# Kernel tuning notes

Hardware: AMD Instinct MI355X
Metric: run time of the kernel (lower is better)

Reference implementation:

```python
import jax, jax.numpy as jnp
import numpy as np

B, T, C = 4, 2048, 1024
H = 16
D = C // H  # head_dim = 64

def setup_inputs() -> dict:
    key = jax.random.key(0)
    ks = jax.random.split(key, 5)
    scale = 0.02
    x = jax.random.normal(ks[0], (B, T, C), dtype=jnp.float32)
    # weights stored [in, out] (transpose of torch Linear layout; same math)
    Wqkv = jax.random.normal(ks[1], (C, 3 * C), dtype=jnp.float32) * scale
    bqkv = jnp.zeros((3 * C,), dtype=jnp.float32)
    Wproj = jax.random.normal(ks[2], (C, C), dtype=jnp.float32) * scale
    bproj = jnp.zeros((C,), dtype=jnp.float32)
    return {"x": x, "Wqkv": Wqkv, "bqkv": bqkv, "Wproj": Wproj, "bproj": bproj}

def reference(x, Wqkv, bqkv, Wproj, bproj):
    Bx, Tx, Cx = x.shape
    qkv = x @ Wqkv + bqkv                      # [B,T,3C]
    q, k, v = jnp.split(qkv, 3, axis=2)
    # [B,T,C] -> [B,H,T,D]
    q = q.reshape(Bx, Tx, H, D).transpose(0, 2, 1, 3)
    k = k.reshape(Bx, Tx, H, D).transpose(0, 2, 1, 3)
    v = v.reshape(Bx, Tx, H, D).transpose(0, 2, 1, 3)
    att = jnp.einsum('bhqd,bhkd->bhqk', q, k) / jnp.sqrt(jnp.float32(D))
    causal = jnp.tril(jnp.ones((Tx, Tx), dtype=bool))
    att = jnp.where(causal, att, jnp.float32(-jnp.inf))
    att = jax.nn.softmax(att, axis=-1)
    y = jnp.einsum('bhqk,bhkd->bhqd', att, v)  # [B,H,T,D]
    y = y.transpose(0, 2, 1, 3).reshape(Bx, Tx, Cx)
    return y @ Wproj + bproj
```

## Files before the change

### kernel.cpp

```cpp
#include <hip/hip_runtime.h>
#include <math.h>

#define Bb 4
#define Tt 2048
#define Cc 1024
#define Hh 16
#define Dd 64
#define QSC 0.18033688011112042f

typedef unsigned short ushort_t;
typedef __attribute__((ext_vector_type(8))) short short8;
typedef __attribute__((ext_vector_type(4))) float floatx4;

typedef unsigned int __attribute__((address_space(1))) u32_as1;
typedef unsigned int __attribute__((address_space(3))) u32_as3;

__device__ __forceinline__ void gld_lds16(const void* g, const void* lds_uniform) {
    __builtin_amdgcn_global_load_lds(
        (const u32_as1*)(unsigned long long)g,
        (u32_as3*)(unsigned int)(unsigned long long)lds_uniform,
        16, 0, 0);
}

__device__ inline ushort_t f2bf(float x) {
    unsigned int u = __float_as_uint(x);
    return (ushort_t)((u + 0x7FFFu + ((u >> 16) & 1u)) >> 16);
}

__device__ __forceinline__ void bar() {
    asm volatile("" ::: "memory");
    __builtin_amdgcn_s_barrier();
    asm volatile("" ::: "memory");
}

__global__ __launch_bounds__(256) void convert_kernel(
    const float* __restrict__ in, ushort_t* __restrict__ out, int n4)
{
    int i = blockIdx.x * 256 + threadIdx.x;
    if (i < n4) {
        float4 v = *(const float4*)&in[i * 4];
        ushort_t o[4] = {f2bf(v.x), f2bf(v.y), f2bf(v.z), f2bf(v.w)};
        *(uint2*)&out[i * 4] = *(uint2*)o;
    }
}

__global__ __launch_bounds__(256) void transpose_kernel(
    const float* __restrict__ W, ushort_t* __restrict__ Wt, int K, int N)
{
    __shared__ ushort_t Ts[16][72];
    const int n0 = blockIdx.x * 64;
    const int k0 = blockIdx.y * 16;
    const int t = threadIdx.x;
#pragma unroll
    for (int i = 0; i < 4; i++) {
        int e = t + i * 256;
        int kl = e >> 6, nl = e & 63;
        Ts[kl][nl] = f2bf(W[(size_t)(k0 + kl) * N + n0 + nl]);
    }
    __syncthreads();
    {
        int nl = t >> 2, kl4 = (t & 3) * 4;
        ushort_t o[4] = {Ts[kl4][nl], Ts[kl4 + 1][nl], Ts[kl4 + 2][nl], Ts[kl4 + 3][nl]};
        *(uint2*)&Wt[(size_t)(n0 + nl) * K + k0 + kl4] = *(uint2*)o;
    }
}

template <bool OUT_BF16, bool SCALE_Q>
__global__ __launch_bounds__(512) void gemm256_kernel(
    const ushort_t* __restrict__ A, const ushort_t* __restrict__ Bt,
    const float* __restrict__ bias, void* __restrict__ Co,
    int M, int N, int K)
{
    __shared__ __align__(16) ushort_t Ls[65536];

    const int tid = threadIdx.x;
    const int lane = tid & 63;
    const int w = tid >> 6;
    const int wm = w >> 2, wn = w & 3;
    const int l = lane & 15, q = lane >> 4;
    const int NT = K >> 6;

    const int n0 = blockIdx.x * 256;
    const int m0 = blockIdx.y * 256;

    const int ln = lane ^ (((lane >> 5) & 1) << 1);
    const ushort_t* Ag = A  + (size_t)(m0 + w * 16 + (ln >> 2)) * K + (ln & 3) * 8;
    const ushort_t* Bg = Bt + (size_t)(n0 + w * 16 + (ln >> 2)) * K + (ln & 3) * 8;

    const int swz = l * 32 + ((q * 8) ^ (((l >> 3) & 1) << 4));

    floatx4 acc[2][2][4][2];
#pragma unroll
    for (int qm = 0; qm < 2; qm++)
#pragma unroll
        for (int qn = 0; qn < 2; qn++)
#pragma unroll
            for (int mf = 0; mf < 4; mf++)
#pragma unroll
                for (int nf = 0; nf < 2; nf++)
                    acc[qm][qn][mf][nf] = (floatx4){0.f, 0.f, 0.f, 0.f};

    short8 af[4][2], bf0[2][2], bf1[2][2];

#define STAGE_(SLOT, MAT, HALF, T, GB) {                                        \
    const ushort_t* _g = (GB) + (size_t)(HALF) * 128 * K + (size_t)(T) * 64;    \
    const ushort_t* _l = &Ls[(SLOT) * 32768 + (MAT) * 16384 + (HALF) * 8192 + w * 1024]; \
    gld_lds16(_g, _l);                                                          \
    gld_lds16(_g + 32, _l + 512); }
#define STAGE_A(SLOT, HALF, T) STAGE_((SLOT), 0, (HALF), (T), Ag)
#define STAGE_B(SLOT, HALF, T) STAGE_((SLOT), 1, (HALF), (T), Bg)

#define LDA(SLOT, QM) {                                                         \
    _Pragma("unroll") for (int mf = 0; mf < 4; mf++)                            \
    _Pragma("unroll") for (int kc = 0; kc < 2; kc++)                            \
        af[mf][kc] = *(const short8*)&Ls[(SLOT) * 32768 + (QM) * 8192 +         \
            ((wm * 4 + mf) * 2 + kc) * 512 + swz]; }

#define LDB(SLOT, QN, DST) {                                                    \
    _Pragma("unroll") for (int nf = 0; nf < 2; nf++)                            \
    _Pragma("unroll") for (int kc = 0; kc < 2; kc++)                            \
        DST[nf][kc] = *(const short8*)&Ls[(SLOT) * 32768 + 16384 + (QN) * 8192 + \
            ((wn * 2 + nf) * 2 + kc) * 512 + swz]; }

#define MM(QM, QN, BF) {                                                        \
    __builtin_amdgcn_s_setprio(1);                                              \
    _Pragma("unroll") for (int kc = 0; kc < 2; kc++)                            \
    _Pragma("unroll") for (int mf = 0; mf < 4; mf++)                            \
    _Pragma("unroll") for (int nf = 0; nf < 2; nf++)                            \
        acc[QM][QN][mf][nf] = __builtin_amdgcn_mfma_f32_16x16x32_bf16(          \
            af[mf][kc], BF[nf][kc], acc[QM][QN][mf][nf], 0, 0, 0);              \
    __builtin_amdgcn_s_setprio(0); }

#define LGKM0() asm volatile("s_waitcnt lgkmcnt(0)" ::: "memory")

    STAGE_A(0, 0, 0); STAGE_B(0, 0, 0); STAGE_B(0, 1, 0); STAGE_A(0, 1, 0);
    if (NT > 1) {
        STAGE_A(1, 0, 1); STAGE_B(1, 0, 1); STAGE_B(1, 1, 1);
        asm volatile("s_waitcnt vmcnt(6)" ::: "memory");
    } else {
        asm volatile("s_waitcnt vmcnt(0)" ::: "memory");
    }
    bar();

    for (int g = 0; g < NT; ++g) {
        const int slot = g & 1;

        LDA(slot, 0);
        LDB(slot, 0, bf0);
        if (g + 1 < NT) STAGE_A(slot ^ 1, 1, g + 1);
        bar();
        LGKM0();
        MM(0, 0, bf0);
        bar();

        LDB(slot, 1, bf1);
        if (g + 2 < NT) STAGE_A(slot, 0, g + 2);
        bar();
        LGKM0();
        MM(0, 1, bf1);
        bar();

        LDA(slot, 1);
        if (g + 2 < NT) STAGE_B(slot, 0, g + 2);
        bar();
        LGKM0();
        MM(1, 1, bf1);
        bar();

        if (g + 2 < NT) STAGE_B(slot, 1, g + 2);
        bar();
        LGKM0();
        MM(1, 0, bf0);
        if (g + 1 < NT) {
            if (g + 2 < NT) asm volatile("s_waitcnt vmcnt(6)" ::: "memory");
            else            asm volatile("s_waitcnt vmcnt(0)" ::: "memory");
            bar();
        }
    }

#pragma unroll
    for (int qn = 0; qn < 2; qn++)
#pragma unroll
        for (int nf = 0; nf < 2; nf++) {
            const int col = n0 + qn * 128 + wn * 32 + nf * 16 + l;
            const float bi = bias[col];
            const float sc = (SCALE_Q && col < 1024) ? QSC : 1.0f;
#pragma unroll
            for (int qm = 0; qm < 2; qm++)
#pragma unroll
                for (int mf = 0; mf < 4; mf++)
#pragma unroll
                    for (int r = 0; r < 4; r++) {
                        const int row = m0 + qm * 128 + wm * 64 + mf * 16 + q * 4 + r;
                        const float v = (acc[qm][qn][mf][nf][r] + bi) * sc;
                        if (OUT_BF16)
                            ((ushort_t*)Co)[(size_t)row * N + col] = f2bf(v);
                        else
                            ((float*)Co)[(size_t)row * N + col] = v;
                    }
        }
#undef STAGE_
#undef STAGE_A
#undef STAGE_B
#undef LDA
#undef LDB
#undef MM
#undef LGKM0
}

__global__ __launch_bounds__(256, 2) void attn_mfma_kernel(
    const ushort_t* __restrict__ qkv, ushort_t* __restrict__ yatt)
{
    __shared__ __align__(16) ushort_t Ks[8 * 512];
    __shared__ __align__(16) ushort_t Vt[80][80];
    __shared__ __align__(16) ushort_t Ps[4][16][80];

    const int tid = threadIdx.x;
    const int lane = tid & 63;
    const int w = tid >> 6;
    const int quad = lane >> 4;
    const int l = lane & 15;

    const int a = blockIdx.x;
    const int q0h[2] = {a * 128, (15 - a) * 128};
    const int bh = blockIdx.y;
    const int b = bh >> 4;
    const int h = bh & 15;
    const size_t base = (size_t)b * Tt * (3 * Cc);
    const int qoff = h * 64;
    const int koff = Cc + h * 64;
    const int voff = 2 * Cc + h * 64;

    for (int i = tid; i < 16 * 80; i += 256)
        Vt[64 + i / 80][i % 80] = 0x3F80;

    short8 Qf[2][2][2];
#pragma unroll
    for (int hf = 0; hf < 2; hf++)
#pragma unroll
        for (int mt = 0; mt < 2; mt++)
#pragma unroll
            for (int kc = 0; kc < 2; kc++)
                Qf[hf][mt][kc] = *(const short8*)&qkv[base
                    + (size_t)(q0h[hf] + mt * 64 + w * 16 + l) * (3 * Cc)
                    + qoff + kc * 32 + quad * 8];

    floatx4 Oacc[2][2][4];
    floatx4 Lacc[2][2];
#pragma unroll
    for (int hf = 0; hf < 2; hf++)
#pragma unroll
        for (int mt = 0; mt < 2; mt++) {
            Lacc[hf][mt] = (floatx4){0.f, 0.f, 0.f, 0.f};
#pragma unroll
            for (int dt = 0; dt < 4; dt++)
                Oacc[hf][mt][dt] = (floatx4){0.f, 0.f, 0.f, 0.f};
        }

    const int srow = tid >> 2;
    const int sd0 = (tid & 3) * 16;
    const int knt = srow >> 4, kl = srow & 15;
    const int kc_s = sd0 >> 5;
    const int qp0 = (sd0 & 31) >> 3;
    const int pcol = (srow & 15) * 4 + (srow >> 4);

    const int ntil = 32 - 2 * a;
    const int ntil_light = 2 * a + 2;

    for (int kt = 0; kt < ntil; kt++) {
        const int kbase = kt * 64;
        __syncthreads();
        {
            const ushort_t* kp = &qkv[base + (size_t)(kbase + srow) * (3 * Cc) + koff + sd0];
            const ushort_t* vp = &qkv[base + (size_t)(kbase + srow) * (3 * Cc) + voff + sd0];
            uint4 kv0 = *(const uint4*)kp;
            uint4 kv1 = *(const uint4*)(kp + 8);
            *(uint4*)&Ks[(knt * 2 + kc_s) * 512 + (qp0 * 16 + kl) * 8] = kv0;
            *(uint4*)&Ks[(knt * 2 + kc_s) * 512 + ((qp0 + 1) * 16 + kl) * 8] = kv1;
            ushort_t tv[16];
            *(uint4*)&tv[0] = *(const uint4*)vp;
            *(uint4*)&tv[8] = *(const uint4*)(vp + 8);
#pragma unroll
            for (int j = 0; j < 16; j++) Vt[sd0 + j][pcol] = tv[j];
        }
        __syncthreads();

        short8 Vf[5][2];
#pragma unroll
        for (int dt = 0; dt < 5; dt++)
#pragma unroll
            for (int kc = 0; kc < 2; kc++)
                Vf[dt][kc] = *(const short8*)&Vt[dt * 16 + l][kc * 32 + quad * 8];

#pragma unroll
        for (int hf = 0; hf < 2; hf++) {
            if (hf == 0 && kt >= ntil_light) continue;
#pragma unroll
            for (int mt = 0; mt < 2; mt++) {
                const int qmin = q0h[hf] + mt * 64 + (w << 4);
                if (kbase > qmin + 15) continue;

                floatx4 S[4];
#pragma unroll
                for (int nt = 0; nt < 4; nt++) S[nt] = (floatx4){0.f, 0.f, 0.f, 0.f};
#pragma unroll
                for (int kc = 0; kc < 2; kc++) {
#pragma unroll
                    for (int nt = 0; nt < 4; nt++) {
                        short8 kf = *(const short8*)&Ks[(nt * 2 + kc) * 512 + lane * 8];
                        S[nt] = __builtin_amdgcn_mfma_f32_16x16x32_bf16(
                            Qf[hf][mt][kc], kf, S[nt], 0, 0, 0);
                    }
                }

                const bool need_mask = (kbase + 63 > qmin);

#pragma unroll
                for (int r = 0; r < 4; r++) {
                    const int qrow = qmin + quad * 4 + r;
                    float e[4];
#pragma unroll
                    for (int nt = 0; nt < 4; nt++) {
                        float s = S[nt][r];
                        if (need_mask && (kbase + nt * 16 + l > qrow)) s = -INFINITY;
                        e[nt] = __builtin_amdgcn_exp2f(s);
                    }
                    unsigned int u0 = __builtin_amdgcn_perm(
                        __float_as_uint(e[1]), __float_as_uint(e[0]), 0x07060302u);
                    unsigned int u1 = __builtin_amdgcn_perm(
                        __float_as_uint(e[3]), __float_as_uint(e[2]), 0x07060302u);
                    uint2 pk; pk.x = u0; pk.y = u1;
                    *(uint2*)&Ps[w][quad * 4 + r][l * 4] = pk;
                }
                asm volatile("" ::: "memory");

                short8 Pa0 = *(const short8*)&Ps[w][l][quad * 8];
                short8 Pa1 = *(const short8*)&Ps[w][l][32 + quad * 8];
#pragma unroll
                for (int dt = 0; dt < 4; dt++) {
                    Oacc[hf][mt][dt] = __builtin_amdgcn_mfma_f32_16x16x32_bf16(
                        Pa0, Vf[dt][0], Oacc[hf][mt][dt], 0, 0, 0);
                    Oacc[hf][mt][dt] = __builtin_amdgcn_mfma_f32_16x16x32_bf16(
                        Pa1, Vf[dt][1], Oacc[hf][mt][dt], 0, 0, 0);
                }
                Lacc[hf][mt] = __builtin_amdgcn_mfma_f32_16x16x32_bf16(
                    Pa0, Vf[4][0], Lacc[hf][mt], 0, 0, 0);
                Lacc[hf][mt] = __builtin_amdgcn_mfma_f32_16x16x32_bf16(
                    Pa1, Vf[4][1], Lacc[hf][mt], 0, 0, 0);
                asm volatile("" ::: "memory");
            }
        }
    }

#pragma unroll
    for (int hf = 0; hf < 2; hf++)
#pragma unroll
        for (int mt = 0; mt < 2; mt++)
#pragma unroll
            for (int r = 0; r < 4; r++) {
                const float rl = 1.f / Lacc[hf][mt][r];
                const int qrow = q0h[hf] + mt * 64 + (w << 4) + quad * 4 + r;
#pragma unroll
                for (int dt = 0; dt < 4; dt++)
                    yatt[(size_t)(b * Tt + qrow) * Cc + h * 64 + dt * 16 + l] =
                        f2bf(Oacc[hf][mt][dt][r] * rl);
            }
}

extern "C" void kernel_launch(void* const* d_in, const int* in_sizes, int n_in,
                              void* d_out, int out_size, void* d_ws, size_t ws_size,
                              hipStream_t stream) {
    const float* x     = (const float*)d_in[0];
    const float* Wqkv  = (const float*)d_in[1];
    const float* bqkv  = (const float*)d_in[2];
    const float* Wproj = (const float*)d_in[3];
    const float* bproj = (const float*)d_in[4];
    float* out = (float*)d_out;

    ushort_t* qkvb   = (ushort_t*)d_ws;
    ushort_t* yattb  = qkvb + (size_t)8192 * 3072;
    ushort_t* xb     = yattb + (size_t)8192 * 1024;
    ushort_t* wqkvt  = xb + (size_t)8192 * 1024;
    ushort_t* wprojt = wqkvt + (size_t)3072 * 1024;

    convert_kernel<<<(8192 * 1024 / 4 + 255) / 256, 256, 0, stream>>>(x, xb, 8192 * 1024 / 4);
    transpose_kernel<<<dim3(3072 / 64, 1024 / 16), 256, 0, stream>>>(Wqkv, wqkvt, 1024, 3072);
    transpose_kernel<<<dim3(1024 / 64, 1024 / 16), 256, 0, stream>>>(Wproj, wprojt, 1024, 1024);

    gemm256_kernel<true, true><<<dim3(3072 / 256, 8192 / 256), 512, 0, stream>>>(
        xb, wqkvt, bqkv, qkvb, 8192, 3072, 1024);
    attn_mfma_kernel<<<dim3(8, Bb * Hh), 256, 0, stream>>>(qkvb, yattb);
    gemm256_kernel<false, false><<<dim3(1024 / 256, 8192 / 256), 512, 0, stream>>>(
        yattb, wprojt, bproj, out, 8192, 1024, 1024);
}
```

Measured before the change: 278.7 us.

## Split attention into one block per query tile, add LDS swizzles and K/V prefetch

Replaces the paired light/heavy query-tile scheme with one 128-row query tile per block, launched heavy-first over a 64x16 grid, and raises launch bounds to 4 blocks per CU. It XOR-swizzles the K, V-transpose and P shared-memory layouts to reduce bank conflicts. It register-prefetches the next K/V tile during compute and raises wave priority around MFMA sections. The aim is better load balance, occupancy and latency hiding, at the cost of more blocks and some index arithmetic. A stray label was also added in the host launch code.

```diff
diff --git a/kernel.cpp b/kernel.cpp
--- a/kernel.cpp
+++ b/kernel.cpp
@@ -208,12 +208,22 @@
 #undef LGKM0
 }
 
-__global__ __launch_bounds__(256, 2) void attn_mfma_kernel(
+__device__ __forceinline__ int ks_swz(int I) {
+    return I ^ (((I >> 8) & 1) * 0x28) ^ (((I >> 9) & 1) * 0x10);
+}
+__device__ __forceinline__ int vt_idx(int row, int col) {
+    return row * 80 + (col ^ ((((row >> 2) ^ (row >> 4)) & 3) << 3));
+}
+__device__ __forceinline__ int ps_idx(int row, int col) {
+    return row * 80 + (col ^ (((row >> 2) & 3) << 3));
+}
+
+__global__ __launch_bounds__(256, 4) void attn_mfma_kernel(
     const ushort_t* __restrict__ qkv, ushort_t* __restrict__ yatt)
 {
     __shared__ __align__(16) ushort_t Ks[8 * 512];
-    __shared__ __align__(16) ushort_t Vt[80][80];
-    __shared__ __align__(16) ushort_t Ps[4][16][80];
+    __shared__ __align__(16) ushort_t Vt[80 * 80];
+    __shared__ __align__(16) ushort_t Ps[4][16 * 80];
 
     const int tid = threadIdx.x;
     const int lane = tid & 63;
@@ -221,9 +231,9 @@
     const int quad = lane >> 4;
     const int l = lane & 15;
 
-    const int a = blockIdx.x;
-    const int q0h[2] = {a * 128, (15 - a) * 128};
-    const int bh = blockIdx.y;
+    const int bh = blockIdx.x;
+    const int j = 15 - (int)blockIdx.y;
+    const int q0 = j * 128;
     const int b = bh >> 4;
     const int h = bh & 15;
     const size_t base = (size_t)b * Tt * (3 * Cc);
@@ -231,31 +241,27 @@
     const int koff = Cc + h * 64;
     const int voff = 2 * Cc + h * 64;
 
-    for (int i = tid; i < 16 * 80; i += 256)
-        Vt[64 + i / 80][i % 80] = 0x3F80;
-
-    short8 Qf[2][2][2];
-#pragma unroll
-    for (int hf = 0; hf < 2; hf++)
-#pragma unroll
-        for (int mt = 0; mt < 2; mt++)
-#pragma unroll
-            for (int kc = 0; kc < 2; kc++)
-                Qf[hf][mt][kc] = *(const short8*)&qkv[base
-                    + (size_t)(q0h[hf] + mt * 64 + w * 16 + l) * (3 * Cc)
-                    + qoff + kc * 32 + quad * 8];
-
-    floatx4 Oacc[2][2][4];
-    floatx4 Lacc[2][2];
-#pragma unroll
-    for (int hf = 0; hf < 2; hf++)
-#pragma unroll
-        for (int mt = 0; mt < 2; mt++) {
-            Lacc[hf][mt] = (floatx4){0.f, 0.f, 0.f, 0.f};
-#pragma unroll
-            for (int dt = 0; dt < 4; dt++)
-                Oacc[hf][mt][dt] = (floatx4){0.f, 0.f, 0.f, 0.f};
-        }
+    for (int i = tid; i < 16 * 64; i += 256)
+        Vt[vt_idx(64 + i / 64, i % 64)] = 0x3F80;
+
+    short8 Qf[2][2];
+#pragma unroll
+    for (int mt = 0; mt < 2; mt++)
+#pragma unroll
+        for (int kc = 0; kc < 2; kc++)
+            Qf[mt][kc] = *(const short8*)&qkv[base
+                + (size_t)(q0 + mt * 64 + w * 16 + l) * (3 * Cc)
+                + qoff + kc * 32 + quad * 8];
+
+    floatx4 Oacc[2][4];
+    floatx4 Lacc[2];
+#pragma unroll
+    for (int mt = 0; mt < 2; mt++) {
+        Lacc[mt] = (floatx4){0.f, 0.f, 0.f, 0.f};
+#pragma unroll
+        for (int dt = 0; dt < 4; dt++)
+            Oacc[mt][dt] = (floatx4){0.f, 0.f, 0.f, 0.f};
+    }
 
     const int srow = tid >> 2;
     const int sd0 = (tid & 3) * 16;
@@ -264,107 +270,119 @@
     const int qp0 = (sd0 & 31) >> 3;
     const int pcol = (srow & 15) * 4 + (srow >> 4);
 
-    const int ntil = 32 - 2 * a;
-    const int ntil_light = 2 * a + 2;
+    const int ntil = 2 * j + 2;
+
+    const ushort_t* kp0 = &qkv[base + (size_t)srow * (3 * Cc) + koff + sd0];
+    const ushort_t* vp0 = &qkv[base + (size_t)srow * (3 * Cc) + voff + sd0];
+
+    uint4 pk0 = *(const uint4*)kp0;
+    uint4 pk1 = *(const uint4*)(kp0 + 8);
+    uint4 pv0 = *(const uint4*)vp0;
+    uint4 pv1 = *(const uint4*)(vp0 + 8);
+
+    const int ksw0 = ks_swz((knt * 2 + kc_s) * 512 + (qp0 * 16 + kl) * 8);
+    const int ksw1 = ks_swz((knt * 2 + kc_s) * 512 + ((qp0 + 1) * 16 + kl) * 8);
 
     for (int kt = 0; kt < ntil; kt++) {
         const int kbase = kt * 64;
         __syncthreads();
+        *(uint4*)&Ks[ksw0] = pk0;
+        *(uint4*)&Ks[ksw1] = pk1;
         {
-            const ushort_t* kp = &qkv[base + (size_t)(kbase + srow) * (3 * Cc) + koff + sd0];
-            const ushort_t* vp = &qkv[base + (size_t)(kbase + srow) * (3 * Cc) + voff + sd0];
-            uint4 kv0 = *(const uint4*)kp;
-            uint4 kv1 = *(const uint4*)(kp + 8);
-            *(uint4*)&Ks[(knt * 2 + kc_s) * 512 + (qp0 * 16 + kl) * 8] = kv0;
-            *(uint4*)&Ks[(knt * 2 + kc_s) * 512 + ((qp0 + 1) * 16 + kl) * 8] = kv1;
             ushort_t tv[16];
-            *(uint4*)&tv[0] = *(const uint4*)vp;
-            *(uint4*)&tv[8] = *(const uint4*)(vp + 8);
-#pragma unroll
-            for (int j = 0; j < 16; j++) Vt[sd0 + j][pcol] = tv[j];
+            *(uint4*)&tv[0] = pv0;
+            *(uint4*)&tv[8] = pv1;
+#pragma unroll
+            for (int t2 = 0; t2 < 16; t2++) Vt[vt_idx(sd0 + t2, pcol)] = tv[t2];
         }
         __syncthreads();
 
+        if (kt + 1 < ntil) {
+            const size_t off = (size_t)(kbase + 64) * (3 * Cc);
+            pk0 = *(const uint4*)(kp0 + off);
+            pk1 = *(const uint4*)(kp0 + off + 8);
+            pv0 = *(const uint4*)(vp0 + off);
+            pv1 = *(const uint4*)(vp0 + off + 8);
+        }
+
         short8 Vf[5][2];
 #pragma unroll
         for (int dt = 0; dt < 5; dt++)
 #pragma unroll
             for (int kc = 0; kc < 2; kc++)
-                Vf[dt][kc] = *(const short8*)&Vt[dt * 16 + l][kc * 32 + quad * 8];
-
-#pragma unroll
-        for (int hf = 0; hf < 2; hf++) {
-            if (hf == 0 && kt >= ntil_light) continue;
-#pragma unroll
-            for (int mt = 0; mt < 2; mt++) {
-                const int qmin = q0h[hf] + mt * 64 + (w << 4);
-                if (kbase > qmin + 15) continue;
-
-                floatx4 S[4];
-#pragma unroll
-                for (int nt = 0; nt < 4; nt++) S[nt] = (floatx4){0.f, 0.f, 0.f, 0.f};
-#pragma unroll
-                for (int kc = 0; kc < 2; kc++) {
-#pragma unroll
-                    for (int nt = 0; nt < 4; nt++) {
-                        short8 kf = *(const short8*)&Ks[(nt * 2 + kc) * 512 + lane * 8];
-                        S[nt] = __builtin_amdgcn_mfma_f32_16x16x32_bf16(
-                            Qf[hf][mt][kc], kf, S[nt], 0, 0, 0);
-                    }
+                Vf[dt][kc] = *(const short8*)&Vt[vt_idx(dt * 16 + l, kc * 32 + quad * 8)];
+
+#pragma unroll
+        for (int mt = 0; mt < 2; mt++) {
+            const int qmin = q0 + mt * 64 + (w << 4);
+            if (kbase > qmin + 15) continue;
+
+            floatx4 S[4];
+#pragma unroll
+            for (int nt = 0; nt < 4; nt++) S[nt] = (floatx4){0.f, 0.f, 0.f, 0.f};
+            __builtin_amdgcn_s_setprio(1);
+#pragma unroll
+            for (int kc = 0; kc < 2; kc++) {
+#pragma unroll
+                for (int nt = 0; nt < 4; nt++) {
+                    short8 kf = *(const short8*)&Ks[ks_swz((nt * 2 + kc) * 512 + lane * 8)];
+                    S[nt] = __builtin_amdgcn_mfma_f32_16x16x32_bf16(
+                        Qf[mt][kc], kf, S[nt], 0, 0, 0);
                 }
-
-                const bool need_mask = (kbase + 63 > qmin);
-
-#pragma unroll
-                for (int r = 0; r < 4; r++) {
-                    const int qrow = qmin + quad * 4 + r;
-                    float e[4];
-#pragma unroll
-                    for (int nt = 0; nt < 4; nt++) {
-                        float s = S[nt][r];
-                        if (need_mask && (kbase + nt * 16 + l > qrow)) s = -INFINITY;
-                        e[nt] = __builtin_amdgcn_exp2f(s);
-                    }
-                    unsigned int u0 = __builtin_amdgcn_perm(
-                        __float_as_uint(e[1]), __float_as_uint(e[0]), 0x07060302u);
-                    unsigned int u1 = __builtin_amdgcn_perm(
-                        __float_as_uint(e[3]), __float_as_uint(e[2]), 0x07060302u);
-                    uint2 pk; pk.x = u0; pk.y = u1;
-                    *(uint2*)&Ps[w][quad * 4 + r][l * 4] = pk;
+            }
+            __builtin_amdgcn_s_setprio(0);
+
+            const bool need_mask = (kbase + 63 > qmin);
+
+#pragma unroll
+            for (int r = 0; r < 4; r++) {
+                const int qrow = qmin + quad * 4 + r;
+                float e[4];
+#pragma unroll
+                for (int nt = 0; nt < 4; nt++) {
+                    float s = S[nt][r];
+                    if (need_mask && (kbase + nt * 16 + l > qrow)) s = -INFINITY;
+                    e[nt] = __builtin_amdgcn_exp2f(s);
                 }
-                asm volatile("" ::: "memory");
-
-                short8 Pa0 = *(const short8*)&Ps[w][l][quad * 8];
-                short8 Pa1 = *(const short8*)&Ps[w][l][32 + quad * 8];
-#pragma unroll
-                for (int dt = 0; dt < 4; dt++) {
-                    Oacc[hf][mt][dt] = __builtin_amdgcn_mfma_f32_16x16x32_bf16(
-                        Pa0, Vf[dt][0], Oacc[hf][mt][dt], 0, 0, 0);
-                    Oacc[hf][mt][dt] = __builtin_amdgcn_mfma_f32_16x16x32_bf16(
-                        Pa1, Vf[dt][1], Oacc[hf][mt][dt], 0, 0, 0);
-                }
-                Lacc[hf][mt] = __builtin_amdgcn_mfma_f32_16x16x32_bf16(
-                    Pa0, Vf[4][0], Lacc[hf][mt], 0, 0, 0);
-                Lacc[hf][mt] = __builtin_amdgcn_mfma_f32_16x16x32_bf16(
-                    Pa1, Vf[4][1], Lacc[hf][mt], 0, 0, 0);
-                asm volatile("" ::: "memory");
+                unsigned int u0 = __builtin_amdgcn_perm(
+                    __float_as_uint(e[1]), __float_as_uint(e[0]), 0x07060302u);
+                unsigned int u1 = __builtin_amdgcn_perm(
+                    __float_as_uint(e[3]), __float_as_uint(e[2]), 0x07060302u);
+                uint2 pk; pk.x = u0; pk.y = u1;
+                *(uint2*)&Ps[w][ps_idx(quad * 4 + r, l * 4)] = pk;
             }
-        }
-    }
-
-#pragma unroll
-    for (int hf = 0; hf < 2; hf++)
-#pragma unroll
-        for (int mt = 0; mt < 2; mt++)
-#pragma unroll
-            for (int r = 0; r < 4; r++) {
-                const float rl = 1.f / Lacc[hf][mt][r];
-                const int qrow = q0h[hf] + mt * 64 + (w << 4) + quad * 4 + r;
-#pragma unroll
-                for (int dt = 0; dt < 4; dt++)
-                    yatt[(size_t)(b * Tt + qrow) * Cc + h * 64 + dt * 16 + l] =
-                        f2bf(Oacc[hf][mt][dt][r] * rl);
+            asm volatile("" ::: "memory");
+
+            short8 Pa0 = *(const short8*)&Ps[w][ps_idx(l, quad * 8)];
+            short8 Pa1 = *(const short8*)&Ps[w][ps_idx(l, 32 + quad * 8)];
+            __builtin_amdgcn_s_setprio(1);
+#pragma unroll
+            for (int dt = 0; dt < 4; dt++) {
+                Oacc[mt][dt] = __builtin_amdgcn_mfma_f32_16x16x32_bf16(
+                    Pa0, Vf[dt][0], Oacc[mt][dt], 0, 0, 0);
+                Oacc[mt][dt] = __builtin_amdgcn_mfma_f32_16x16x32_bf16(
+                    Pa1, Vf[dt][1], Oacc[mt][dt], 0, 0, 0);
             }
+            Lacc[mt] = __builtin_amdgcn_mfma_f32_16x16x32_bf16(
+                Pa0, Vf[4][0], Lacc[mt], 0, 0, 0);
+            Lacc[mt] = __builtin_amdgcn_mfma_f32_16x16x32_bf16(
+                Pa1, Vf[4][1], Lacc[mt], 0, 0, 0);
+            __builtin_amdgcn_s_setprio(0);
+            asm volatile("" ::: "memory");
+        }
+    }
+
+#pragma unroll
+    for (int mt = 0; mt < 2; mt++)
+#pragma unroll
+        for (int r = 0; r < 4; r++) {
+            const float rl = 1.f / Lacc[mt][r];
+            const int qrow = q0 + mt * 64 + (w << 4) + quad * 4 + r;
+#pragma unroll
+            for (int dt = 0; dt < 4; dt++)
+                yatt[(size_t)(b * Tt + qrow) * Cc + h * 64 + dt * 16 + l] =
+                    f2bf(Oacc[mt][dt][r] * rl);
+        }
 }
 
 extern "C" void kernel_launch(void* const* d_in, const int* in_sizes, int n_in,
@@ -387,9 +405,10 @@
     transpose_kernel<<<dim3(3072 / 64, 1024 / 16), 256, 0, stream>>>(Wqkv, wqkvt, 1024, 3072);
     transpose_kernel<<<dim3(1024 / 64, 1024 / 16), 256, 0, stream>>>(Wproj, wprojt, 1024, 1024);
 
+    gemm_bf16_launch:
     gemm256_kernel<true, true><<<dim3(3072 / 256, 8192 / 256), 512, 0, stream>>>(
         xb, wqkvt, bqkv, qkvb, 8192, 3072, 1024);
-    attn_mfma_kernel<<<dim3(8, Bb * Hh), 256, 0, stream>>>(qkvb, yattb);
+    attn_mfma_kernel<<<dim3(64, 16), 256, 0, stream>>>(qkvb, yattb);
     gemm256_kernel<false, false><<<dim3(1024 / 256, 8192 / 256), 512, 0, stream>>>(
         yattb, wprojt, bproj, out, 8192, 1024, 1024);
 }
```

New measurement: 442.0 us. +58.6%, slower.
